# Kernel optimization log

Hardware: AMD Instinct MI355X
Metric: run time of the kernel (lower is better)

Reference implementation:

```python
import jax, jax.numpy as jnp
import numpy as np

DIM = 192
HEADS = 6
WS = 8          # window size
SHIFT = 4       # shift size
HIDDEN = 384    # mlp hidden = 2.0 * dim
EPS = 1e-5


def _rel_pos_index(ws):
    # static [N, N] int index into the (2*ws-1)^2 bias table
    coords = np.stack(np.meshgrid(np.arange(ws), np.arange(ws), indexing='ij')).reshape(2, -1)
    rel = (coords[:, :, None] - coords[:, None, :]).transpose(1, 2, 0)
    rel[..., 0] += ws - 1
    rel[..., 1] += ws - 1
    rel[..., 0] *= 2 * ws - 1
    return rel.sum(-1)


def _attn_mask(hp, wp, ws, shift):
    # static shift-window mask: [nW, N, N], 0 or -100
    img = np.zeros((hp, wp))
    sl = (slice(0, -ws), slice(-ws, -shift), slice(-shift, None))
    cnt = 0
    for hs in sl:
        for wsl in sl:
            img[hs, wsl] = cnt
            cnt += 1
    m = img.reshape(hp // ws, ws, wp // ws, ws).transpose(0, 2, 1, 3).reshape(-1, ws * ws)
    diff = m[:, None, :] - m[:, :, None]
    return np.where(diff != 0, -100.0, 0.0).astype(np.float32)


def _ln(x, g, b):
    mu = x.mean(-1, keepdims=True)
    var = ((x - mu) ** 2).mean(-1, keepdims=True)
    return (x - mu) * jax.lax.rsqrt(var + EPS) * g + b


def setup_inputs() -> dict:
    key = jax.random.key(0)
    ks = jax.random.split(key, 6)
    B, H, W, C = 4, 224, 224, DIM
    return {
        'x': jax.random.normal(ks[0], (B, H * W, C), jnp.float32),
        'norm1_g': jnp.ones((C,), jnp.float32),
        'norm1_b': jnp.zeros((C,), jnp.float32),
        'qkv_w': jax.random.normal(ks[1], (C, 3 * C), jnp.float32) * 0.02,
        'qkv_b': jnp.zeros((3 * C,), jnp.float32),
        'proj_w': jax.random.normal(ks[2], (C, C), jnp.float32) * 0.02,
        'proj_b': jnp.zeros((C,), jnp.float32),
        'rel_bias_table': jax.random.normal(ks[3], ((2 * WS - 1) ** 2, HEADS), jnp.float32) * 0.02,
        'norm2_g': jnp.ones((C,), jnp.float32),
        'norm2_b': jnp.zeros((C,), jnp.float32),
        'fc1_w': jax.random.normal(ks[4], (C, HIDDEN), jnp.float32) * 0.02,
        'fc1_b': jnp.zeros((HIDDEN,), jnp.float32),
        'fc2_w': jax.random.normal(ks[5], (HIDDEN, C), jnp.float32) * 0.02,
        'fc2_b': jnp.zeros((C,), jnp.float32),
        'height': 224,
        'width': 224,
    }


def reference(x, norm1_g, norm1_b, qkv_w, qkv_b, proj_w, proj_b, rel_bias_table,
              norm2_g, norm2_b, fc1_w, fc1_b, fc2_w, fc2_b, height, width):
    B, T, C = x.shape
    dh = C // HEADS
    scale = dh ** (-0.5)
    shortcut = x

    xw = _ln(x, norm1_g, norm1_b).reshape(B, height, width, C)
    pad_h = (WS - height % WS) % WS
    pad_w = (WS - width % WS) % WS
    if pad_h > 0 or pad_w > 0:
        xw = jnp.pad(xw, ((0, 0), (0, pad_h), (0, pad_w), (0, 0)))
    Hp, Wp = height + pad_h, width + pad_w

    if SHIFT > 0:
        xs = jnp.roll(xw, (-SHIFT, -SHIFT), axis=(1, 2))
        mask = jnp.asarray(_attn_mask(Hp, Wp, WS, SHIFT))  # [nW, N, N]
    else:
        xs, mask = xw, None

    N = WS * WS
    # window partition -> [B*nW, N, C]
    xwin = xs.reshape(B, Hp // WS, WS, Wp // WS, WS, C).transpose(0, 1, 3, 2, 4, 5).reshape(-1, N, C)

    qkv = (xwin @ qkv_w + qkv_b).reshape(-1, N, 3, HEADS, dh).transpose(2, 0, 3, 1, 4)
    q, k, v = qkv[0] * scale, qkv[1], qkv[2]          # [B*nW, H, N, dh]
    attn = jnp.einsum('whnd,whmd->whnm', q, k)         # [B*nW, H, N, N]

    idx = jnp.asarray(_rel_pos_index(WS).reshape(-1))
    bias = rel_bias_table[idx].reshape(N, N, HEADS).transpose(2, 0, 1)  # [H, N, N]
    attn = attn + bias[None]

    if mask is not None:
        nW = mask.shape[0]
        attn = attn.reshape(-1, nW, HEADS, N, N) + mask[None, :, None]
        attn = attn.reshape(-1, HEADS, N, N)

    attn = jax.nn.softmax(attn, axis=-1)
    out = jnp.einsum('whnm,whmd->wnhd', attn, v).reshape(-1, N, C)
    out = out @ proj_w + proj_b

    # window reverse -> [B, Hp, Wp, C]
    out = out.reshape(B, Hp // WS, Wp // WS, WS, WS, C).transpose(0, 1, 3, 2, 4, 5).reshape(B, Hp, Wp, C)
    if SHIFT > 0:
        out = jnp.roll(out, (SHIFT, SHIFT), axis=(1, 2))
    if pad_h > 0 or pad_w > 0:
        out = out[:, :height, :width, :]

    x = shortcut + out.reshape(B, height * width, C)
    h = _ln(x, norm2_g, norm2_b)
    h = jax.nn.gelu(h @ fc1_w + fc1_b, approximate=False) @ fc2_w + fc2_b
    return x + h
```

## Files before the change

### kernel.cpp

```cpp
#include <hip/hip_runtime.h>
#include <math.h>

#define T_TOT   200704
#define C_DIM   192
#define HEADS   6
#define DH      32
#define NTOK    64
#define NWIN    3136
#define HID     384
#define IMG     224
#define NSIDE   28
#define WPI     784
#define QSCALE  0.17677669529663687f

typedef unsigned short ushortT;
typedef short bf16x8 __attribute__((ext_vector_type(8)));
typedef float f32x4 __attribute__((ext_vector_type(4)));

__device__ __forceinline__ float bf_lo(unsigned u){ return __uint_as_float(u << 16); }
__device__ __forceinline__ float bf_hi(unsigned u){ return __uint_as_float(u & 0xFFFF0000u); }
__device__ __forceinline__ unsigned short f2bf(float f){
    unsigned u = __float_as_uint(f);
    u += 0x7FFFu + ((u >> 16) & 1u);
    return (unsigned short)(u >> 16);
}
__device__ __forceinline__ unsigned pack2(float a, float b){
    return (unsigned)f2bf(a) | ((unsigned)f2bf(b) << 16);
}

__global__ void k_wprep(const float* __restrict__ w, unsigned short* __restrict__ o, int K, int N)
{
    int idx = blockIdx.x * 256 + threadIdx.x;
    if (idx >= K * N) return;
    int n = idx / K, k = idx - n * K;
    o[idx] = f2bf(w[(size_t)k * N + n]);
}

__global__ void k_bmprep(const float* __restrict__ table, float* __restrict__ bmT)
{
    int idx = blockIdx.x * 256 + threadIdx.x;
    int q = idx & 63, m = (idx >> 6) & 63;
    int head = (idx >> 12) % HEADS, type = idx / (64 * 64 * HEADS);
    int rq = q >> 3, cq = q & 7, rm = m >> 3, cm = m & 7;
    float b = table[((rq - rm + 7) * 15 + (cq - cm + 7)) * HEADS + head];
    int th = type >> 1, tw = type & 1;
    int lq = (th ? (rq >= 4 ? 2 : 1) : 0) * 3 + (tw ? (cq >= 4 ? 2 : 1) : 0);
    int lm = (th ? (rm >= 4 ? 2 : 1) : 0) * 3 + (tw ? (cm >= 4 ? 2 : 1) : 0);
    bmT[idx] = b + ((lq != lm) ? -100.f : 0.f);
}

__global__ void k_ln1_win(const float* __restrict__ x, const float* __restrict__ g,
                          const float* __restrict__ bta, unsigned short* __restrict__ xwin)
{
    int t    = blockIdx.x * 4 + (threadIdx.x >> 6);
    int lane = threadIdx.x & 63;
    int win = t >> 6, n = t & 63;
    int bimg = win / WPI, w2 = win % WPI;
    int wi = w2 / NSIDE, wj = w2 % NSIDE;
    int r = n >> 3, c = n & 7;
    int hs = wi * 8 + r + 4; if (hs >= IMG) hs -= IMG;
    int ws = wj * 8 + c + 4; if (ws >= IMG) ws -= IMG;
    int s = bimg * (IMG*IMG) + hs * IMG + ws;
    const float* xp = x + (size_t)s * C_DIM + lane * 3;
    float v0 = xp[0], v1 = xp[1], v2 = xp[2];
    float sum = v0 + v1 + v2;
    float sq  = v0*v0 + v1*v1 + v2*v2;
    #pragma unroll
    for (int m = 1; m < 64; m <<= 1){ sum += __shfl_xor(sum, m); sq += __shfl_xor(sq, m); }
    float mu = sum * (1.f/192.f);
    float var = sq * (1.f/192.f) - mu*mu;
    float rs = rsqrtf(var + 1e-5f);
    int j = lane * 3;
    unsigned short* op = xwin + (size_t)t * C_DIM + j;
    op[0] = f2bf((v0-mu)*rs*g[j]   + bta[j]);
    op[1] = f2bf((v1-mu)*rs*g[j+1] + bta[j+1]);
    op[2] = f2bf((v2-mu)*rs*g[j+2] + bta[j+2]);
}

template<int KTOT>
__device__ __forceinline__ void mfma_tile(const unsigned short* __restrict__ A,
                                          const unsigned short* __restrict__ Wt,
                                          int t0, int n0,
                                          f32x4 acc[4][2],
                                          unsigned short* As, unsigned short* Bs)
{
    const int tid = threadIdx.x;
    const int lane = tid & 63, wid = tid >> 6;
    const int wm = wid >> 1, wn = wid & 1;
    const int lr = lane & 15, lk = (lane >> 4) << 3;
    #pragma unroll
    for (int i = 0; i < 4; i++)
        #pragma unroll
        for (int j = 0; j < 2; j++)
            acc[i][j] = (f32x4){0.f, 0.f, 0.f, 0.f};

    const int arow = tid >> 1, asoff = (tid & 1) << 4;

    for (int k0 = 0; k0 < KTOT; k0 += 32){
        __syncthreads();
        {
            const unsigned short* ga = A + (size_t)(t0 + arow)*KTOT + k0 + asoff;
            *(uint4*)&As[arow*40 + asoff]     = *(const uint4*)(ga);
            *(uint4*)&As[arow*40 + asoff + 8] = *(const uint4*)(ga + 8);
            if (tid < 128){
                const unsigned short* gb = Wt + (size_t)(n0 + arow)*KTOT + k0 + asoff;
                *(uint4*)&Bs[arow*40 + asoff]     = *(const uint4*)(gb);
                *(uint4*)&Bs[arow*40 + asoff + 8] = *(const uint4*)(gb + 8);
            }
        }
        __syncthreads();
        bf16x8 b0 = *(const bf16x8*)&Bs[(wn*32 +      lr)*40 + lk];
        bf16x8 b1 = *(const bf16x8*)&Bs[(wn*32 + 16 + lr)*40 + lk];
        #pragma unroll
        for (int mf = 0; mf < 4; mf++){
            bf16x8 a = *(const bf16x8*)&As[(wm*64 + mf*16 + lr)*40 + lk];
            acc[mf][0] = __builtin_amdgcn_mfma_f32_16x16x32_bf16(a, b0, acc[mf][0], 0, 0, 0);
            acc[mf][1] = __builtin_amdgcn_mfma_f32_16x16x32_bf16(a, b1, acc[mf][1], 0, 0, 0);
        }
    }
}

__global__ void k_qkv_m(const unsigned short* __restrict__ xwin, const unsigned short* __restrict__ wt,
                        const float* __restrict__ bias,
                        unsigned short* __restrict__ q, unsigned short* __restrict__ k,
                        unsigned short* __restrict__ v)
{
    __shared__ __align__(16) unsigned short As[128*40];
    __shared__ __align__(16) unsigned short Bs[64*40];
    int t0 = blockIdx.x * 128, n0 = blockIdx.y * 64;
    f32x4 acc[4][2];
    mfma_tile<C_DIM>(xwin, wt, t0, n0, acc, As, Bs);

    const int tid = threadIdx.x, lane = tid & 63, wid = tid >> 6;
    const int wm = wid >> 1, wn = wid & 1, lr = lane & 15;
    int win = blockIdx.x * 2 + wm;
    #pragma unroll
    for (int nf = 0; nf < 2; nf++){
        int c = n0 + wn*32 + nf*16 + lr;
        float b = bias[c];
        int which = c / C_DIM, cc = c % C_DIM;
        unsigned short* dst = (which == 0) ? q : (which == 1) ? k : v;
        float sc = (which == 0) ? QSCALE : 1.f;
        int head = cc >> 5, d = cc & 31;
        unsigned short* dp = dst + ((size_t)(win*HEADS + head) * NTOK) * DH + d;
        #pragma unroll
        for (int mf = 0; mf < 4; mf++){
            #pragma unroll
            for (int r = 0; r < 4; r++){
                int ntok = mf*16 + ((lane >> 4) << 2) + r;
                dp[ntok*DH] = f2bf((acc[mf][nf][r] + b) * sc);
            }
        }
    }
}

__global__ void k_attn_mfma(const unsigned short* __restrict__ q, const unsigned short* __restrict__ k,
                            const unsigned short* __restrict__ v, const float* __restrict__ bmT,
                            unsigned short* __restrict__ attn_o)
{
    __shared__ __align__(16) unsigned short Vt[4][32*72];
    __shared__ __align__(16) unsigned short Ps[4][64*72];
    const int tid = threadIdx.x, lane = tid & 63, wid = tid >> 6;
    const int wh = blockIdx.x * 4 + wid;
    const int head = wh % HEADS, win = wh / HEADS;
    const int w2 = win % WPI;
    const int type = ((w2 / NSIDE) == 27 ? 2 : 0) + ((w2 % NSIDE) == 27 ? 1 : 0);
    const size_t base = (size_t)wh * (NTOK * DH);
    const int lr = lane & 15, lg = lane >> 4;

    {
        const uint4* vp = (const uint4*)(v + base + lane * DH);
        uint4 va = vp[0], vb = vp[1], vc = vp[2], vd = vp[3];
        unsigned short* dst = &Vt[wid][lane];
        unsigned w0[8] = {va.x, va.y, va.z, va.w, vb.x, vb.y, vb.z, vb.w};
        #pragma unroll
        for (int j = 0; j < 8; j++){
            dst[(2*j)*72]   = (unsigned short)(w0[j] & 0xFFFFu);
            dst[(2*j+1)*72] = (unsigned short)(w0[j] >> 16);
        }
        unsigned w1[8] = {vc.x, vc.y, vc.z, vc.w, vd.x, vd.y, vd.z, vd.w};
        #pragma unroll
        for (int j = 0; j < 8; j++){
            dst[(16+2*j)*72]   = (unsigned short)(w1[j] & 0xFFFFu);
            dst[(16+2*j+1)*72] = (unsigned short)(w1[j] >> 16);
        }
    }

    bf16x8 aq[4], bk[4];
    {
        const unsigned short* qg = q + base + lr * DH + (lg << 3);
        const unsigned short* kg = k + base + lr * DH + (lg << 3);
        #pragma unroll
        for (int i = 0; i < 4; i++){
            aq[i] = *(const bf16x8*)(qg + i * 16 * DH);
            bk[i] = *(const bf16x8*)(kg + i * 16 * DH);
        }
    }

    f32x4 acc[4][4];
    #pragma unroll
    for (int mi = 0; mi < 4; mi++)
        #pragma unroll
        for (int ni = 0; ni < 4; ni++)
            acc[mi][ni] = __builtin_amdgcn_mfma_f32_16x16x32_bf16(aq[mi], bk[ni],
                              (f32x4){0.f,0.f,0.f,0.f}, 0, 0, 0);

    const float* bmBase = bmT + ((size_t)(type * HEADS + head) * 64) * 64;
    #pragma unroll
    for (int mi = 0; mi < 4; mi++)
        #pragma unroll
        for (int ni = 0; ni < 4; ni++){
            float4 bm = *(const float4*)(bmBase + (lr + 16*ni)*64 + lg*4 + 16*mi);
            acc[mi][ni][0] += bm.x; acc[mi][ni][1] += bm.y;
            acc[mi][ni][2] += bm.z; acc[mi][ni][3] += bm.w;
        }

    #pragma unroll
    for (int mi = 0; mi < 4; mi++){
        #pragma unroll
        for (int r = 0; r < 4; r++){
            float mx = fmaxf(fmaxf(acc[mi][0][r], acc[mi][1][r]),
                             fmaxf(acc[mi][2][r], acc[mi][3][r]));
            mx = fmaxf(mx, __shfl_xor(mx, 1));
            mx = fmaxf(mx, __shfl_xor(mx, 2));
            mx = fmaxf(mx, __shfl_xor(mx, 4));
            mx = fmaxf(mx, __shfl_xor(mx, 8));
            float e0 = __expf(acc[mi][0][r] - mx);
            float e1 = __expf(acc[mi][1][r] - mx);
            float e2 = __expf(acc[mi][2][r] - mx);
            float e3 = __expf(acc[mi][3][r] - mx);
            float sum = e0 + e1 + e2 + e3;
            sum += __shfl_xor(sum, 1);
            sum += __shfl_xor(sum, 2);
            sum += __shfl_xor(sum, 4);
            sum += __shfl_xor(sum, 8);
            float inv = 1.f / sum;
            int row = lg*4 + r + 16*mi;
            unsigned short* pr = &Ps[wid][row*72 + lr];
            pr[0]  = f2bf(e0 * inv);
            pr[16] = f2bf(e1 * inv);
            pr[32] = f2bf(e2 * inv);
            pr[48] = f2bf(e3 * inv);
        }
    }

    f32x4 o[4][2];
    #pragma unroll
    for (int mi = 0; mi < 4; mi++)
        #pragma unroll
        for (int ni = 0; ni < 2; ni++)
            o[mi][ni] = (f32x4){0.f,0.f,0.f,0.f};
    #pragma unroll
    for (int kb = 0; kb < 2; kb++){
        bf16x8 ap[4], bv[2];
        #pragma unroll
        for (int mi = 0; mi < 4; mi++)
            ap[mi] = *(const bf16x8*)&Ps[wid][(lr + 16*mi)*72 + (lg<<3) + 32*kb];
        #pragma unroll
        for (int ni = 0; ni < 2; ni++)
            bv[ni] = *(const bf16x8*)&Vt[wid][(lr + 16*ni)*72 + (lg<<3) + 32*kb];
        #pragma unroll
        for (int mi = 0; mi < 4; mi++)
            #pragma unroll
            for (int ni = 0; ni < 2; ni++)
                o[mi][ni] = __builtin_amdgcn_mfma_f32_16x16x32_bf16(ap[mi], bv[ni], o[mi][ni], 0, 0, 0);
    }

    unsigned short* ob = attn_o + ((size_t)win * NTOK) * C_DIM + head * DH;
    #pragma unroll
    for (int mi = 0; mi < 4; mi++)
        #pragma unroll
        for (int ni = 0; ni < 2; ni++)
            #pragma unroll
            for (int r = 0; r < 4; r++){
                int row = lg*4 + r + 16*mi;
                ob[(size_t)row * C_DIM + lr + 16*ni] = f2bf(o[mi][ni][r]);
            }
}

__global__ void k_proj_m(const unsigned short* __restrict__ ain, const unsigned short* __restrict__ wt,
                         const float* __restrict__ bias, const float* __restrict__ x,
                         float* __restrict__ out)
{
    __shared__ __align__(16) unsigned short As[128*40];
    __shared__ __align__(16) unsigned short Bs[64*40];
    int t0 = blockIdx.x * 128, n0 = blockIdx.y * 64;
    f32x4 acc[4][2];
    mfma_tile<C_DIM>(ain, wt, t0, n0, acc, As, Bs);

    const int tid = threadIdx.x, lane = tid & 63, wid = tid >> 6;
    const int wm = wid >> 1, wn = wid & 1, lr = lane & 15;
    float b0 = bias[n0 + wn*32 + lr];
    float b1 = bias[n0 + wn*32 + 16 + lr];
    #pragma unroll
    for (int mf = 0; mf < 4; mf++){
        #pragma unroll
        for (int r = 0; r < 4; r++){
            int t = t0 + wm*64 + mf*16 + ((lane >> 4) << 2) + r;
            int win = t >> 6, n = t & 63;
            int bimg = win / WPI, w2 = win % WPI;
            int wi = w2 / NSIDE, wj = w2 % NSIDE;
            int rr = n >> 3, cc = n & 7;
            int hf = wi*8 + rr + 4; if (hf >= IMG) hf -= IMG;
            int wf = wj*8 + cc + 4; if (wf >= IMG) wf -= IMG;
            size_t s = ((size_t)bimg*(IMG*IMG) + hf*IMG + wf) * C_DIM;
            int c0 = n0 + wn*32 + lr;
            out[s + c0]      = x[s + c0]      + acc[mf][0][r] + b0;
            out[s + c0 + 16] = x[s + c0 + 16] + acc[mf][1][r] + b1;
        }
    }
}

#define XS_STR 200
#define H1_STR 392
#define O_STR  196
__global__ void k_mlp(float* __restrict__ out,
                      const float* __restrict__ g, const float* __restrict__ bta,
                      const unsigned short* __restrict__ w1, const float* __restrict__ b1,
                      const unsigned short* __restrict__ w2, const float* __restrict__ b2)
{
    __shared__ __align__(16) unsigned short H1u[32*H1_STR];
    unsigned short* Xs = H1u;
    float* O = (float*)H1u;
    const int tid = threadIdx.x, lane = tid & 63, wid = tid >> 6;
    const int lr = lane & 15, lg = lane >> 4;
    const int t0 = blockIdx.x * 32;

    {
        int row = tid >> 3, part = tid & 7;
        const float* xp = out + (size_t)(t0 + row) * C_DIM + part * 24;
        float vals[24];
        float sum = 0.f, sq = 0.f;
        #pragma unroll
        for (int j = 0; j < 6; j++){
            float4 v4 = *(const float4*)(xp + j*4);
            vals[j*4+0] = v4.x; vals[j*4+1] = v4.y; vals[j*4+2] = v4.z; vals[j*4+3] = v4.w;
            sum += v4.x + v4.y + v4.z + v4.w;
            sq  += v4.x*v4.x + v4.y*v4.y + v4.z*v4.z + v4.w*v4.w;
        }
        sum += __shfl_xor(sum, 1); sq += __shfl_xor(sq, 1);
        sum += __shfl_xor(sum, 2); sq += __shfl_xor(sq, 2);
        sum += __shfl_xor(sum, 4); sq += __shfl_xor(sq, 4);
        float mu = sum * (1.f/192.f);
        float var = sq * (1.f/192.f) - mu*mu;
        float rs = rsqrtf(var + 1e-5f);
        int c0 = part * 24;
        #pragma unroll
        for (int j = 0; j < 3; j++){
            int c = c0 + j*8;
            float4 ga = *(const float4*)(g + c), gb = *(const float4*)(g + c + 4);
            float4 ba = *(const float4*)(bta + c), bb = *(const float4*)(bta + c + 4);
            unsigned short tmp[8];
            tmp[0] = f2bf((vals[j*8+0]-mu)*rs*ga.x + ba.x);
            tmp[1] = f2bf((vals[j*8+1]-mu)*rs*ga.y + ba.y);
            tmp[2] = f2bf((vals[j*8+2]-mu)*rs*ga.z + ba.z);
            tmp[3] = f2bf((vals[j*8+3]-mu)*rs*ga.w + ba.w);
            tmp[4] = f2bf((vals[j*8+4]-mu)*rs*gb.x + bb.x);
            tmp[5] = f2bf((vals[j*8+5]-mu)*rs*gb.y + bb.y);
            tmp[6] = f2bf((vals[j*8+6]-mu)*rs*gb.z + bb.z);
            tmp[7] = f2bf((vals[j*8+7]-mu)*rs*gb.w + bb.w);
            *(uint4*)&Xs[row*XS_STR + c] = *(uint4*)tmp;
        }
    }
    __syncthreads();

    f32x4 acc1[6][2];
    {
        #pragma unroll
        for (int mf = 0; mf < 6; mf++)
            #pragma unroll
            for (int nf = 0; nf < 2; nf++)
                acc1[mf][nf] = (f32x4){0.f,0.f,0.f,0.f};
        #pragma unroll
        for (int k0 = 0; k0 < C_DIM; k0 += 32){
            bf16x8 a[6], b[2];
            #pragma unroll
            for (int mf = 0; mf < 6; mf++)
                a[mf] = *(const bf16x8*)(w1 + (size_t)(wid*96 + mf*16 + lr)*C_DIM + k0 + lg*8);
            #pragma unroll
            for (int nf = 0; nf < 2; nf++)
                b[nf] = *(const bf16x8*)&Xs[(nf*16 + lr)*XS_STR + k0 + lg*8];
            #pragma unroll
            for (int mf = 0; mf < 6; mf++)
                #pragma unroll
                for (int nf = 0; nf < 2; nf++)
                    acc1[mf][nf] = __builtin_amdgcn_mfma_f32_16x16x32_bf16(a[mf], b[nf], acc1[mf][nf], 0, 0, 0);
        }
    }
    __syncthreads();

    {
        #pragma unroll
        for (int mf = 0; mf < 6; mf++){
            int hc = wid*96 + mf*16 + lg*4;
            float4 bb = *(const float4*)(b1 + hc);
            float bias[4] = {bb.x, bb.y, bb.z, bb.w};
            #pragma unroll
            for (int nf = 0; nf < 2; nf++){
                int token = nf*16 + lr;
                float gl[4];
                #pragma unroll
                for (int r = 0; r < 4; r++){
                    float u = acc1[mf][nf][r] + bias[r];
                    gl[r] = 0.5f*u*(1.f + erff(u*0.70710678118654752f));
                }
                uint2 pk; pk.x = pack2(gl[0], gl[1]); pk.y = pack2(gl[2], gl[3]);
                *(uint2*)&H1u[token*H1_STR + hc] = pk;
            }
        }
    }
    __syncthreads();

    f32x4 acc2[2][3];
    {
        #pragma unroll
        for (int rf = 0; rf < 2; rf++)
            #pragma unroll
            for (int cf = 0; cf < 3; cf++)
                acc2[rf][cf] = (f32x4){0.f,0.f,0.f,0.f};
        #pragma unroll
        for (int k0 = 0; k0 < HID; k0 += 32){
            bf16x8 a[2], b[3];
            #pragma unroll
            for (int rf = 0; rf < 2; rf++)
                a[rf] = *(const bf16x8*)&H1u[(rf*16 + lr)*H1_STR + k0 + lg*8];
            #pragma unroll
            for (int cf = 0; cf < 3; cf++)
                b[cf] = *(const bf16x8*)(w2 + (size_t)(wid*48 + cf*16 + lr)*HID + k0 + lg*8);
            #pragma unroll
            for (int rf = 0; rf < 2; rf++)
                #pragma unroll
                for (int cf = 0; cf < 3; cf++)
                    acc2[rf][cf] = __builtin_amdgcn_mfma_f32_16x16x32_bf16(a[rf], b[cf], acc2[rf][cf], 0, 0, 0);
        }
    }
    __syncthreads();

    #pragma unroll
    for (int cf = 0; cf < 3; cf++){
        int c = wid*48 + cf*16 + lr;
        float bias = b2[c];
        #pragma unroll
        for (int rf = 0; rf < 2; rf++)
            #pragma unroll
            for (int r = 0; r < 4; r++)
                O[(rf*16 + lg*4 + r)*O_STR + c] = acc2[rf][cf][r] + bias;
    }
    __syncthreads();

    {
        int row = tid >> 3, part = tid & 7;
        float* op = out + (size_t)(t0 + row) * C_DIM;
        const float* Or = O + row * O_STR;
        #pragma unroll
        for (int j = 0; j < 6; j++){
            int c = part*4 + j*32;
            float4 add = *(const float4*)&Or[c];
            float4 old = *(const float4*)&op[c];
            old.x += add.x; old.y += add.y; old.z += add.z; old.w += add.w;
            *(float4*)&op[c] = old;
        }
    }
}

extern "C" void kernel_launch(void* const* d_in, const int* in_sizes, int n_in,
                              void* d_out, int out_size, void* d_ws, size_t ws_size,
                              hipStream_t stream)
{
    const float* x       = (const float*)d_in[0];
    const float* n1g     = (const float*)d_in[1];
    const float* n1b     = (const float*)d_in[2];
    const float* qkv_w   = (const float*)d_in[3];
    const float* qkv_b   = (const float*)d_in[4];
    const float* proj_w  = (const float*)d_in[5];
    const float* proj_b  = (const float*)d_in[6];
    const float* rtab    = (const float*)d_in[7];
    const float* n2g     = (const float*)d_in[8];
    const float* n2b     = (const float*)d_in[9];
    const float* fc1_w   = (const float*)d_in[10];
    const float* fc1_b   = (const float*)d_in[11];
    const float* fc2_w   = (const float*)d_in[12];
    const float* fc2_b   = (const float*)d_in[13];
    float* out = (float*)d_out;

    char* wsb = (char*)d_ws;
    const size_t SZ = (size_t)T_TOT * C_DIM * 2;
    unsigned short* xwin = (unsigned short*)(wsb);
    unsigned short* qb   = (unsigned short*)(wsb + SZ);
    unsigned short* kb   = (unsigned short*)(wsb + 2*SZ);
    unsigned short* vb   = (unsigned short*)(wsb + 3*SZ);
    unsigned short* wt_qkv  = (unsigned short*)(wsb + 4*SZ);
    unsigned short* wt_proj = wt_qkv + 576*192;
    unsigned short* wt_fc1  = wt_proj + 192*192;
    unsigned short* wt_fc2  = wt_fc1 + 384*192;
    float*          bmT     = (float*)(wt_fc2 + 384*192);
    unsigned short* attn_o = xwin;

    k_wprep<<<(192*576 + 255)/256, 256, 0, stream>>>(qkv_w, wt_qkv, 192, 576);
    k_wprep<<<(192*192 + 255)/256, 256, 0, stream>>>(proj_w, wt_proj, 192, 192);
    k_wprep<<<(192*384 + 255)/256, 256, 0, stream>>>(fc1_w, wt_fc1, 192, 384);
    k_wprep<<<(384*192 + 255)/256, 256, 0, stream>>>(fc2_w, wt_fc2, 384, 192);
    k_bmprep<<<(4*HEADS*64*64)/256, 256, 0, stream>>>(rtab, bmT);

    k_ln1_win<<<T_TOT/4, 256, 0, stream>>>(x, n1g, n1b, xwin);
    k_qkv_m<<<dim3(T_TOT/128, 9), 256, 0, stream>>>(xwin, wt_qkv, qkv_b, qb, kb, vb);
    k_attn_mfma<<<NWIN*HEADS/4, 256, 0, stream>>>(qb, kb, vb, bmT, attn_o);
    k_proj_m<<<dim3(T_TOT/128, 3), 256, 0, stream>>>(attn_o, wt_proj, proj_b, x, out);
    k_mlp<<<T_TOT/32, 256, 0, stream>>>(out, n2g, n2b, wt_fc1, fc1_b, wt_fc2, fc2_b);
}
```

Baseline: 733.5 us.

## Fuse LayerNorm1 with QKV projection into one per-window kernel

Replaces the separate LN1+window-partition kernel and the tiled QKV GEMM with a single kernel per window. Each block normalizes its 64 tokens into LDS as bf16 and computes all 576 QKV outputs from there, reading weights directly from global memory. This removes the bf16 xwin round trip through HBM and one launch, and vectorizes the LN loads. In exchange the B operand is no longer staged in LDS, so weight traffic per block rises, and the smaller grid (one block per window) may lower occupancy.

```diff
diff --git a/kernel.cpp b/kernel.cpp
--- a/kernel.cpp
+++ b/kernel.cpp
@@ -49,107 +49,98 @@
     bmT[idx] = b + ((lq != lm) ? -100.f : 0.f);
 }
 
-__global__ void k_ln1_win(const float* __restrict__ x, const float* __restrict__ g,
-                          const float* __restrict__ bta, unsigned short* __restrict__ xwin)
-{
-    int t    = blockIdx.x * 4 + (threadIdx.x >> 6);
-    int lane = threadIdx.x & 63;
-    int win = t >> 6, n = t & 63;
-    int bimg = win / WPI, w2 = win % WPI;
-    int wi = w2 / NSIDE, wj = w2 % NSIDE;
-    int r = n >> 3, c = n & 7;
-    int hs = wi * 8 + r + 4; if (hs >= IMG) hs -= IMG;
-    int ws = wj * 8 + c + 4; if (ws >= IMG) ws -= IMG;
-    int s = bimg * (IMG*IMG) + hs * IMG + ws;
-    const float* xp = x + (size_t)s * C_DIM + lane * 3;
-    float v0 = xp[0], v1 = xp[1], v2 = xp[2];
-    float sum = v0 + v1 + v2;
-    float sq  = v0*v0 + v1*v1 + v2*v2;
-    #pragma unroll
-    for (int m = 1; m < 64; m <<= 1){ sum += __shfl_xor(sum, m); sq += __shfl_xor(sq, m); }
-    float mu = sum * (1.f/192.f);
-    float var = sq * (1.f/192.f) - mu*mu;
-    float rs = rsqrtf(var + 1e-5f);
-    int j = lane * 3;
-    unsigned short* op = xwin + (size_t)t * C_DIM + j;
-    op[0] = f2bf((v0-mu)*rs*g[j]   + bta[j]);
-    op[1] = f2bf((v1-mu)*rs*g[j+1] + bta[j+1]);
-    op[2] = f2bf((v2-mu)*rs*g[j+2] + bta[j+2]);
-}
-
-template<int KTOT>
-__device__ __forceinline__ void mfma_tile(const unsigned short* __restrict__ A,
-                                          const unsigned short* __restrict__ Wt,
-                                          int t0, int n0,
-                                          f32x4 acc[4][2],
-                                          unsigned short* As, unsigned short* Bs)
-{
-    const int tid = threadIdx.x;
-    const int lane = tid & 63, wid = tid >> 6;
-    const int wm = wid >> 1, wn = wid & 1;
-    const int lr = lane & 15, lk = (lane >> 4) << 3;
-    #pragma unroll
-    for (int i = 0; i < 4; i++)
-        #pragma unroll
-        for (int j = 0; j < 2; j++)
-            acc[i][j] = (f32x4){0.f, 0.f, 0.f, 0.f};
-
-    const int arow = tid >> 1, asoff = (tid & 1) << 4;
-
-    for (int k0 = 0; k0 < KTOT; k0 += 32){
-        __syncthreads();
-        {
-            const unsigned short* ga = A + (size_t)(t0 + arow)*KTOT + k0 + asoff;
-            *(uint4*)&As[arow*40 + asoff]     = *(const uint4*)(ga);
-            *(uint4*)&As[arow*40 + asoff + 8] = *(const uint4*)(ga + 8);
-            if (tid < 128){
-                const unsigned short* gb = Wt + (size_t)(n0 + arow)*KTOT + k0 + asoff;
-                *(uint4*)&Bs[arow*40 + asoff]     = *(const uint4*)(gb);
-                *(uint4*)&Bs[arow*40 + asoff + 8] = *(const uint4*)(gb + 8);
-            }
-        }
-        __syncthreads();
-        bf16x8 b0 = *(const bf16x8*)&Bs[(wn*32 +      lr)*40 + lk];
-        bf16x8 b1 = *(const bf16x8*)&Bs[(wn*32 + 16 + lr)*40 + lk];
-        #pragma unroll
-        for (int mf = 0; mf < 4; mf++){
-            bf16x8 a = *(const bf16x8*)&As[(wm*64 + mf*16 + lr)*40 + lk];
-            acc[mf][0] = __builtin_amdgcn_mfma_f32_16x16x32_bf16(a, b0, acc[mf][0], 0, 0, 0);
-            acc[mf][1] = __builtin_amdgcn_mfma_f32_16x16x32_bf16(a, b1, acc[mf][1], 0, 0, 0);
-        }
-    }
-}
-
-__global__ void k_qkv_m(const unsigned short* __restrict__ xwin, const unsigned short* __restrict__ wt,
-                        const float* __restrict__ bias,
-                        unsigned short* __restrict__ q, unsigned short* __restrict__ k,
-                        unsigned short* __restrict__ v)
-{
-    __shared__ __align__(16) unsigned short As[128*40];
-    __shared__ __align__(16) unsigned short Bs[64*40];
-    int t0 = blockIdx.x * 128, n0 = blockIdx.y * 64;
-    f32x4 acc[4][2];
-    mfma_tile<C_DIM>(xwin, wt, t0, n0, acc, As, Bs);
-
+__global__ void k_ln1qkv(const float* __restrict__ x, const float* __restrict__ g,
+                         const float* __restrict__ bta,
+                         const unsigned short* __restrict__ wt, const float* __restrict__ bias,
+                         unsigned short* __restrict__ q, unsigned short* __restrict__ k,
+                         unsigned short* __restrict__ v)
+{
+    __shared__ __align__(16) unsigned short As[64*200];
     const int tid = threadIdx.x, lane = tid & 63, wid = tid >> 6;
-    const int wm = wid >> 1, wn = wid & 1, lr = lane & 15;
-    int win = blockIdx.x * 2 + wm;
-    #pragma unroll
-    for (int nf = 0; nf < 2; nf++){
-        int c = n0 + wn*32 + nf*16 + lr;
-        float b = bias[c];
-        int which = c / C_DIM, cc = c % C_DIM;
-        unsigned short* dst = (which == 0) ? q : (which == 1) ? k : v;
-        float sc = (which == 0) ? QSCALE : 1.f;
-        int head = cc >> 5, d = cc & 31;
-        unsigned short* dp = dst + ((size_t)(win*HEADS + head) * NTOK) * DH + d;
-        #pragma unroll
-        for (int mf = 0; mf < 4; mf++){
-            #pragma unroll
-            for (int r = 0; r < 4; r++){
-                int ntok = mf*16 + ((lane >> 4) << 2) + r;
-                dp[ntok*DH] = f2bf((acc[mf][nf][r] + b) * sc);
-            }
+    const int lr = lane & 15, lg = lane >> 4;
+    const int win = blockIdx.x;
+
+    {
+        int n = tid >> 2, part = tid & 3;
+        int bimg = win / WPI, w2 = win % WPI;
+        int wi = w2 / NSIDE, wj = w2 % NSIDE;
+        int r = n >> 3, c = n & 7;
+        int hs = wi * 8 + r + 4; if (hs >= IMG) hs -= IMG;
+        int ws = wj * 8 + c + 4; if (ws >= IMG) ws -= IMG;
+        size_t s = ((size_t)bimg * (IMG*IMG) + hs * IMG + ws) * C_DIM;
+        const float* xp = x + s + part * 48;
+        float vals[48];
+        float sum = 0.f, sq = 0.f;
+        #pragma unroll
+        for (int j = 0; j < 12; j++){
+            float4 v4 = *(const float4*)(xp + j*4);
+            vals[j*4+0] = v4.x; vals[j*4+1] = v4.y; vals[j*4+2] = v4.z; vals[j*4+3] = v4.w;
+            sum += v4.x + v4.y + v4.z + v4.w;
+            sq  += v4.x*v4.x + v4.y*v4.y + v4.z*v4.z + v4.w*v4.w;
+        }
+        sum += __shfl_xor(sum, 1); sq += __shfl_xor(sq, 1);
+        sum += __shfl_xor(sum, 2); sq += __shfl_xor(sq, 2);
+        float mu = sum * (1.f/192.f);
+        float var = sq * (1.f/192.f) - mu*mu;
+        float rs = rsqrtf(var + 1e-5f);
+        int c0 = part * 48;
+        #pragma unroll
+        for (int j = 0; j < 6; j++){
+            int cc = c0 + j*8;
+            float4 ga = *(const float4*)(g + cc), gb = *(const float4*)(g + cc + 4);
+            float4 ba = *(const float4*)(bta + cc), bb = *(const float4*)(bta + cc + 4);
+            unsigned short tmp[8];
+            tmp[0] = f2bf((vals[j*8+0]-mu)*rs*ga.x + ba.x);
+            tmp[1] = f2bf((vals[j*8+1]-mu)*rs*ga.y + ba.y);
+            tmp[2] = f2bf((vals[j*8+2]-mu)*rs*ga.z + ba.z);
+            tmp[3] = f2bf((vals[j*8+3]-mu)*rs*ga.w + ba.w);
+            tmp[4] = f2bf((vals[j*8+4]-mu)*rs*gb.x + bb.x);
+            tmp[5] = f2bf((vals[j*8+5]-mu)*rs*gb.y + bb.y);
+            tmp[6] = f2bf((vals[j*8+6]-mu)*rs*gb.z + bb.z);
+            tmp[7] = f2bf((vals[j*8+7]-mu)*rs*gb.w + bb.w);
+            *(uint4*)&As[n*200 + cc] = *(uint4*)tmp;
+        }
+    }
+    __syncthreads();
+
+    #pragma unroll
+    for (int chunk = 0; chunk < 3; chunk++){
+        f32x4 acc[3][4];
+        #pragma unroll
+        for (int nf = 0; nf < 3; nf++)
+            #pragma unroll
+            for (int mf = 0; mf < 4; mf++)
+                acc[nf][mf] = (f32x4){0.f,0.f,0.f,0.f};
+        #pragma unroll
+        for (int k0 = 0; k0 < C_DIM; k0 += 32){
+            bf16x8 a[4], b[3];
+            #pragma unroll
+            for (int mf = 0; mf < 4; mf++)
+                a[mf] = *(const bf16x8*)&As[(mf*16 + lr)*200 + k0 + lg*8];
+            #pragma unroll
+            for (int nf = 0; nf < 3; nf++)
+                b[nf] = *(const bf16x8*)(wt + (size_t)(chunk*192 + wid*48 + nf*16 + lr)*C_DIM + k0 + lg*8);
+            #pragma unroll
+            for (int nf = 0; nf < 3; nf++)
+                #pragma unroll
+                for (int mf = 0; mf < 4; mf++)
+                    acc[nf][mf] = __builtin_amdgcn_mfma_f32_16x16x32_bf16(a[mf], b[nf], acc[nf][mf], 0, 0, 0);
+        }
+        unsigned short* dst = (chunk == 0) ? q : (chunk == 1) ? k : v;
+        float sc = (chunk == 0) ? QSCALE : 1.f;
+        #pragma unroll
+        for (int nf = 0; nf < 3; nf++){
+            int cc = wid*48 + nf*16 + lr;
+            float b = bias[chunk*192 + cc];
+            int head = cc >> 5, d = cc & 31;
+            unsigned short* dp = dst + ((size_t)(win*HEADS + head) * NTOK) * DH + d;
+            #pragma unroll
+            for (int mf = 0; mf < 4; mf++)
+                #pragma unroll
+                for (int r = 0; r < 4; r++){
+                    int ntok = mf*16 + lg*4 + r;
+                    dp[ntok*DH] = f2bf((acc[nf][mf][r] + b) * sc);
+                }
         }
     }
 }
@@ -278,6 +269,49 @@
             }
 }
 
+template<int KTOT>
+__device__ __forceinline__ void mfma_tile(const unsigned short* __restrict__ A,
+                                          const unsigned short* __restrict__ Wt,
+                                          int t0, int n0,
+                                          f32x4 acc[4][2],
+                                          unsigned short* As, unsigned short* Bs)
+{
+    const int tid = threadIdx.x;
+    const int lane = tid & 63, wid = tid >> 6;
+    const int wm = wid >> 1, wn = wid & 1;
+    const int lr = lane & 15, lk = (lane >> 4) << 3;
+    #pragma unroll
+    for (int i = 0; i < 4; i++)
+        #pragma unroll
+        for (int j = 0; j < 2; j++)
+            acc[i][j] = (f32x4){0.f, 0.f, 0.f, 0.f};
+
+    const int arow = tid >> 1, asoff = (tid & 1) << 4;
+
+    for (int k0 = 0; k0 < KTOT; k0 += 32){
+        __syncthreads();
+        {
+            const unsigned short* ga = A + (size_t)(t0 + arow)*KTOT + k0 + asoff;
+            *(uint4*)&As[arow*40 + asoff]     = *(const uint4*)(ga);
+            *(uint4*)&As[arow*40 + asoff + 8] = *(const uint4*)(ga + 8);
+            if (tid < 128){
+                const unsigned short* gb = Wt + (size_t)(n0 + arow)*KTOT + k0 + asoff;
+                *(uint4*)&Bs[arow*40 + asoff]     = *(const uint4*)(gb);
+                *(uint4*)&Bs[arow*40 + asoff + 8] = *(const uint4*)(gb + 8);
+            }
+        }
+        __syncthreads();
+        bf16x8 b0 = *(const bf16x8*)&Bs[(wn*32 +      lr)*40 + lk];
+        bf16x8 b1 = *(const bf16x8*)&Bs[(wn*32 + 16 + lr)*40 + lk];
+        #pragma unroll
+        for (int mf = 0; mf < 4; mf++){
+            bf16x8 a = *(const bf16x8*)&As[(wm*64 + mf*16 + lr)*40 + lk];
+            acc[mf][0] = __builtin_amdgcn_mfma_f32_16x16x32_bf16(a, b0, acc[mf][0], 0, 0, 0);
+            acc[mf][1] = __builtin_amdgcn_mfma_f32_16x16x32_bf16(a, b1, acc[mf][1], 0, 0, 0);
+        }
+    }
+}
+
 __global__ void k_proj_m(const unsigned short* __restrict__ ain, const unsigned short* __restrict__ wt,
                          const float* __restrict__ bias, const float* __restrict__ x,
                          float* __restrict__ out)
@@ -485,7 +519,7 @@
 
     char* wsb = (char*)d_ws;
     const size_t SZ = (size_t)T_TOT * C_DIM * 2;
-    unsigned short* xwin = (unsigned short*)(wsb);
+    unsigned short* attn_o = (unsigned short*)(wsb);
     unsigned short* qb   = (unsigned short*)(wsb + SZ);
     unsigned short* kb   = (unsigned short*)(wsb + 2*SZ);
     unsigned short* vb   = (unsigned short*)(wsb + 3*SZ);
@@ -494,7 +528,6 @@
     unsigned short* wt_fc1  = wt_proj + 192*192;
     unsigned short* wt_fc2  = wt_fc1 + 384*192;
     float*          bmT     = (float*)(wt_fc2 + 384*192);
-    unsigned short* attn_o = xwin;
 
     k_wprep<<<(192*576 + 255)/256, 256, 0, stream>>>(qkv_w, wt_qkv, 192, 576);
     k_wprep<<<(192*192 + 255)/256, 256, 0, stream>>>(proj_w, wt_proj, 192, 192);
@@ -502,8 +535,7 @@
     k_wprep<<<(384*192 + 255)/256, 256, 0, stream>>>(fc2_w, wt_fc2, 384, 192);
     k_bmprep<<<(4*HEADS*64*64)/256, 256, 0, stream>>>(rtab, bmT);
 
-    k_ln1_win<<<T_TOT/4, 256, 0, stream>>>(x, n1g, n1b, xwin);
-    k_qkv_m<<<dim3(T_TOT/128, 9), 256, 0, stream>>>(xwin, wt_qkv, qkv_b, qb, kb, vb);
+    k_ln1qkv<<<NWIN, 256, 0, stream>>>(x, n1g, n1b, wt_qkv, qkv_b, qb, kb, vb);
     k_attn_mfma<<<NWIN*HEADS/4, 256, 0, stream>>>(qb, kb, vb, bmT, attn_o);
     k_proj_m<<<dim3(T_TOT/128, 3), 256, 0, stream>>>(attn_o, wt_proj, proj_b, x, out);
     k_mlp<<<T_TOT/32, 256, 0, stream>>>(out, n2g, n2b, wt_fc1, fc1_b, wt_fc2, fc2_b);
```

After: 760.7 us. +3.7%, slower.
